# Performance work log

Measured on AMD Instinct MI355X. Metric: run time of the kernel, lower is better.

Reference implementation:

```python
import jax, jax.numpy as jnp
import numpy as np

N = 4_000_000   # points at level d
SIDE = 1024     # coordinate range per axis
HALF = SIDE // 2  # parent coord range


def setup_inputs() -> dict:
    key = jax.random.key(0)
    k1, k2 = jax.random.split(key)
    xyz = jax.random.randint(k1, (N, 3), 0, SIDE, dtype=jnp.int32)
    b = (jnp.arange(N, dtype=jnp.int32) % 4)[:, None]  # 4 batches
    coords = jnp.concatenate([b, xyz], axis=1)          # (N,4): [b,x,y,z]
    kernel = jnp.ones((8,), dtype=jnp.float32)          # frozen all-ones 2x2x2 conv weights
    return {"coords": coords, "kernel": kernel}


def _fog(coords, kernel):
    # pos(): occupancy code 2**(x%2 + 2*y%2 + 4*z%2)
    bits = coords[:, 1:4] & 1                       # (N,3)
    off = bits[:, 0] + 2 * bits[:, 1] + 4 * bits[:, 2]  # (N,) child offset in 2x2x2 window
    pos = jnp.exp2(off.astype(jnp.float32))         # (N,) code in {1,2,4,...,128}
    contrib = pos * kernel[off]                     # per-offset conv weight (all ones)
    # stride-2 conv: parent voxel = floor(xyz/2); linearize (b,z,y,x) into a key
    parent = coords[:, 1:4] >> 1                    # (N,3)
    keys = (((coords[:, 0].astype(jnp.int64) * HALF + parent[:, 2]) * HALF
             + parent[:, 1]) * HALF + parent[:, 0])
    ukeys, inv = jnp.unique(keys, return_inverse=True, size=N, fill_value=-1)
    feats = jax.ops.segment_sum(contrib, inv, num_segments=N)[:, None]  # (N,1)
    # decode padded unique keys back to coords; pad slots -> -1
    px = (ukeys % HALF).astype(jnp.int32)
    py = ((ukeys // HALF) % HALF).astype(jnp.int32)
    pz = ((ukeys // (HALF * HALF)) % HALF).astype(jnp.int32)
    pb = (ukeys // (HALF * HALF * HALF)).astype(jnp.int32)
    valid = (ukeys >= 0)[:, None]
    coords_out = jnp.where(valid, jnp.stack([pb, px, py, pz], axis=1), -1)
    return coords_out, feats


def reference(coords, kernel):
    return _fog(coords, kernel)
```

## Files before the change

kernel.cpp:

```cpp
#include <hip/hip_runtime.h>
#include <stdint.h>

typedef unsigned int u32;
typedef unsigned long long u64;

#define LBITS  14
#define LMASK  ((1u << LBITS) - 1u)
#define NBUCK  (1u << (29 - LBITS))
#define BWORDS (1u << (LBITS - 5))
#define WPL    (BWORDS / 64)
#define WOPAD  (BWORDS + BWORDS / 32)
#define FCAP   192
#define BPB    4
#define TILE_A 4096
#define RPT    (TILE_A / 256)
#define S2     8
#define CAP2   2304
#define RPT2   (CAP2 / 256)
#define RECV   4
#define SCAN_ELEM 2048

__device__ __forceinline__ u32 woidx(u32 w) { return w + (w >> 5); }

__device__ __forceinline__ void wsync() {
    asm volatile("s_waitcnt lgkmcnt(0)" ::: "memory");
}

__device__ __forceinline__ u32 make_key(int4 c) {
    return ((((u32)c.x * 512u + ((u32)c.w >> 1)) * 512u + ((u32)c.z >> 1)) * 512u)
           + ((u32)c.y >> 1);
}

__global__ void __launch_bounds__(256) phase_a(const int4* __restrict__ coords,
        u32* __restrict__ linrec, u32* __restrict__ histmat, int n, u32 NT) {
    __shared__ u32 h[4 * 256];
    u32 t = threadIdx.x, wave = t >> 6;
    for (u32 j = t; j < 1024u; j += 256u) h[j] = 0u;
    __syncthreads();
    u32 base = blockIdx.x * TILE_A;
    u32 m = min((u32)TILE_A, (u32)n - base);
    for (u32 j = t; j < m; j += 256u) {
        int4 c = coords[base + j];
        u32 key = make_key(c);
        u32 off = ((u32)c.y & 1u) | (((u32)c.z & 1u) << 1) | (((u32)c.w & 1u) << 2);
        u32 rec = (key << 3) | off;
        linrec[base + j] = rec;
        atomicAdd(&h[wave * 256u + (rec >> 24)], 1u);
    }
    __syncthreads();
    histmat[t * NT + blockIdx.x] = h[t] + h[256u + t] + h[512u + t] + h[768u + t];
}

__global__ void scan_reduce(const u32* __restrict__ data, u32* __restrict__ partial, u32 G) {
    __shared__ u32 s[256];
    u32 t = threadIdx.x;
    u32 base = blockIdx.x * SCAN_ELEM + t * 8u;
    u32 sum = 0;
    #pragma unroll
    for (int j = 0; j < 8; ++j) { u32 idx = base + j; if (idx < G) sum += data[idx]; }
    s[t] = sum; __syncthreads();
    for (int d = 128; d > 0; d >>= 1) { if ((int)t < d) s[t] += s[t + d]; __syncthreads(); }
    if (t == 0) partial[blockIdx.x] = s[0];
}

__global__ void scan_apply2(const u32* __restrict__ data, u32* __restrict__ out,
                            const u32* __restrict__ partial, u32 G, u32 NB,
                            u32* __restrict__ total) {
    __shared__ u32 s[256];
    __shared__ u32 pb[2];
    u32 t = threadIdx.x;
    u32 p = (t < NB) ? partial[t] : 0u;
    u32 pbef = (t < blockIdx.x) ? p : 0u;
    s[t] = pbef; __syncthreads();
    for (int d = 128; d > 0; d >>= 1) { if ((int)t < d) s[t] += s[t + d]; __syncthreads(); }
    if (t == 0) pb[0] = s[0];
    __syncthreads();
    if (total) {
        s[t] = p; __syncthreads();
        for (int d = 128; d > 0; d >>= 1) { if ((int)t < d) s[t] += s[t + d]; __syncthreads(); }
        if (t == 0) pb[1] = s[0];
        __syncthreads();
        if (blockIdx.x == NB - 1u && t == 0u) total[0] = pb[1];
    }
    u32 base = blockIdx.x * SCAN_ELEM + t * 8u;
    u32 v[8]; u32 sum = 0;
    #pragma unroll
    for (int j = 0; j < 8; ++j) {
        u32 idx = base + j;
        v[j] = (idx < G) ? data[idx] : 0u;
        sum += v[j];
    }
    s[t] = sum; __syncthreads();
    for (int d = 1; d < 256; d <<= 1) {
        u32 add = (t >= (u32)d) ? s[t - d] : 0u;
        __syncthreads(); s[t] += add; __syncthreads();
    }
    u32 run = s[t] - sum + pb[0];
    #pragma unroll
    for (int j = 0; j < 8; ++j) {
        u32 idx = base + j;
        if (idx < G) { u32 x = v[j]; out[idx] = run; run += x; }
    }
}

__global__ void __launch_bounds__(256) part1(const u32* __restrict__ linrec,
        const u32* __restrict__ histmat, u32* __restrict__ tmp, int n, u32 NT) {
    __shared__ u32 stage[TILE_A];
    __shared__ u32 lcur[256];
    __shared__ u32 gb[256];
    __shared__ u32 wtot[4];
    u32 t = threadIdx.x, wave = t >> 6, lane = t & 63u;
    u32 base = blockIdx.x * TILE_A;
    u32 m = min((u32)TILE_A, (u32)n - base);
    lcur[t] = 0u;
    __syncthreads();
    u32 recv[RPT];
    #pragma unroll
    for (int k = 0; k < RPT; ++k) {
        u32 j = (u32)k * 256u + t;
        if (j < m) {
            u32 rec = linrec[base + j];
            recv[k] = rec;
            atomicAdd(&lcur[rec >> 24], 1u);
        }
    }
    __syncthreads();
    u32 v = lcur[t];
    u32 incl = v;
    #pragma unroll
    for (int d = 1; d < 64; d <<= 1) {
        u32 x = __shfl_up(incl, d);
        if ((int)lane >= d) incl += x;
    }
    if (lane == 63u) wtot[wave] = incl;
    __syncthreads();
    u32 off = (wave > 0u ? wtot[0] : 0u) + (wave > 1u ? wtot[1] : 0u)
            + (wave > 2u ? wtot[2] : 0u);
    u32 excl = off + incl - v;
    lcur[t] = excl;
    gb[t] = histmat[t * NT + blockIdx.x] - excl;
    __syncthreads();
    #pragma unroll
    for (int k = 0; k < RPT; ++k) {
        u32 j = (u32)k * 256u + t;
        if (j < m) {
            u32 rec = recv[k];
            u32 pos = atomicAdd(&lcur[rec >> 24], 1u);
            stage[pos] = rec;
        }
    }
    __syncthreads();
    for (u32 j = t; j < m; j += 256u) {
        u32 rec = stage[j];
        tmp[gb[rec >> 24] + j] = rec;
    }
}

__global__ void __launch_bounds__(256) part2a(const u32* __restrict__ tmp,
        const u32* __restrict__ histmat, u32* __restrict__ hist2, int n, u32 NT) {
    __shared__ u32 h[4 * 128];
    u32 t = threadIdx.x, wave = t >> 6;
    u32 c = blockIdx.x / S2, s = blockIdx.x % S2;
    for (u32 j = t; j < 512u; j += 256u) h[j] = 0u;
    __syncthreads();
    u32 cs = histmat[c * NT];
    u32 ce = (c == 255u) ? (u32)n : histmat[(c + 1u) * NT];
    u32 L = ce - cs;
    u32 lo = cs + L * s / S2, hi = cs + L * (s + 1u) / S2;
    for (u32 i = lo + t; i < hi; i += 256u)
        atomicAdd(&h[wave * 128u + ((tmp[i] >> 17) & 127u)], 1u);
    __syncthreads();
    if (t < 128u)
        hist2[((c * 128u + t) * S2) + s] = h[t] + h[128u + t] + h[256u + t] + h[384u + t];
}

__global__ void __launch_bounds__(256) part2b(const u32* __restrict__ tmp,
        const u32* __restrict__ histmat, const u32* __restrict__ hist2,
        u32* __restrict__ buckrec, int n, u32 NT) {
    __shared__ u32 stage[CAP2];
    __shared__ u32 lcur[128];
    __shared__ u32 gb[128];
    __shared__ u32 wtot[2];
    u32 t = threadIdx.x, lane = t & 63u;
    u32 c = blockIdx.x / S2, s = blockIdx.x % S2;
    u32 cs = histmat[c * NT];
    u32 ce = (c == 255u) ? (u32)n : histmat[(c + 1u) * NT];
    u32 L = ce - cs;
    u32 lo = cs + L * s / S2, hi = cs + L * (s + 1u) / S2;
    u32 cnt = hi - lo;
    if (cnt <= (u32)CAP2) {
        if (t < 128u) lcur[t] = 0u;
        __syncthreads();
        u32 recv[RPT2];
        #pragma unroll
        for (int k = 0; k < RPT2; ++k) {
            u32 j = (u32)k * 256u + t;
            if (j < cnt) {
                u32 rec = tmp[lo + j];
                recv[k] = rec;
                atomicAdd(&lcur[(rec >> 17) & 127u], 1u);
            }
        }
        __syncthreads();
        u32 v = 0, incl = 0, excl = 0;
        if (t < 128u) {
            v = lcur[t];
            incl = v;
            #pragma unroll
            for (int d = 1; d < 64; d <<= 1) {
                u32 x = __shfl_up(incl, d);
                if ((int)lane >= d) incl += x;
            }
            if (lane == 63u) wtot[t >> 6] = incl;
        }
        __syncthreads();
        if (t < 128u) {
            u32 off = (t >= 64u) ? wtot[0] : 0u;
            excl = off + incl - v;
            lcur[t] = excl;
            gb[t] = hist2[((c * 128u + t) * S2) + s] - excl;
        }
        __syncthreads();
        #pragma unroll
        for (int k = 0; k < RPT2; ++k) {
            u32 j = (u32)k * 256u + t;
            if (j < cnt) {
                u32 rec = recv[k];
                u32 pos = atomicAdd(&lcur[(rec >> 17) & 127u], 1u);
                stage[pos] = rec;
            }
        }
        __syncthreads();
        for (u32 j = t; j < cnt; j += 256u) {
            u32 rec = stage[j];
            buckrec[gb[(rec >> 17) & 127u] + j] = rec;
        }
    } else {
        if (t < 128u) lcur[t] = hist2[((c * 128u + t) * S2) + s];
        __syncthreads();
        for (u32 i = lo + t; i < hi; i += 256u) {
            u32 rec = tmp[i];
            u32 pos = atomicAdd(&lcur[(rec >> 17) & 127u], 1u);
            buckrec[pos] = rec;
        }
    }
}

__global__ void __launch_bounds__(256) pass_count(const u32* __restrict__ buckrec,
        const u32* __restrict__ hist2, u32* __restrict__ ucount, int n) {
    __shared__ u32 bm[BPB][WOPAD];
    u32 wave = threadIdx.x >> 6, lane = threadIdx.x & 63u;
    u32 bucket = blockIdx.x * BPB + wave;
    u32* B = bm[wave];
    #pragma unroll
    for (int j = 0; j < WPL; ++j) B[woidx(lane * WPL + j)] = 0u;
    wsync();
    u32 start = hist2[bucket * S2];
    u32 end = (bucket + 1u < NBUCK) ? hist2[(bucket + 1u) * S2] : (u32)n;
    for (u32 i = start + lane; i < end; i += 64u) {
        u32 lk = (buckrec[i] >> 3) & LMASK;
        atomicOr(&B[woidx(lk >> 5)], 1u << (lk & 31u));
    }
    wsync();
    u32 sum = 0;
    #pragma unroll
    for (int j = 0; j < WPL; ++j) sum += __popc(B[woidx(lane * WPL + j)]);
    #pragma unroll
    for (int d = 1; d < 64; d <<= 1) sum += __shfl_xor(sum, d);
    if (lane == 0u) ucount[bucket] = sum;
}

__global__ void __launch_bounds__(256) pass_emit(const u32* __restrict__ buckrec,
        const u32* __restrict__ hist2, const u32* __restrict__ ubase,
        const float* __restrict__ kern, float4* __restrict__ rows,
        float* __restrict__ feats, int n) {
    __shared__ u32 bm[BPB][WOPAD];
    __shared__ u32 wofW[BPB][BWORDS];
    __shared__ float fl[BPB][FCAP];
    __shared__ float ksc[BPB][8];
    u32 wave = threadIdx.x >> 6, lane = threadIdx.x & 63u;
    u32 bucket = blockIdx.x * BPB + wave;
    u32* B = bm[wave];
    u32* W = wofW[wave];
    float* F = fl[wave];
    #pragma unroll
    for (int j = 0; j < WPL; ++j) B[woidx(lane * WPL + j)] = 0u;
    #pragma unroll
    for (u32 j = lane; j < FCAP; j += 64u) F[j] = 0.f;
    if (lane < 8u) ksc[wave][lane] = (float)(1u << lane) * kern[lane];
    wsync();
    u32 start = hist2[bucket * S2];
    u32 end = (bucket + 1u < NBUCK) ? hist2[(bucket + 1u) * S2] : (u32)n;
    u32 cnt = end - start;
    u32 recv[RECV];
    #pragma unroll
    for (int k = 0; k < RECV; ++k) {
        u32 idx = (u32)k * 64u + lane;
        if (idx < cnt) {
            u32 rec = buckrec[start + idx];
            recv[k] = rec;
            u32 lk = (rec >> 3) & LMASK;
            atomicOr(&B[woidx(lk >> 5)], 1u << (lk & 31u));
        }
    }
    for (u32 i = start + (u32)RECV * 64u + lane; i < end; i += 64u) {
        u32 lk = (buckrec[i] >> 3) & LMASK;
        atomicOr(&B[woidx(lk >> 5)], 1u << (lk & 31u));
    }
    wsync();
    u32 wv[WPL]; u32 pc[WPL]; u32 sum = 0;
    #pragma unroll
    for (int j = 0; j < WPL; ++j) {
        wv[j] = B[woidx(lane * WPL + j)];
        pc[j] = __popc(wv[j]);
        sum += pc[j];
    }
    u32 incl = sum;
    #pragma unroll
    for (int d = 1; d < 64; d <<= 1) {
        u32 tt = __shfl_up(incl, d);
        if ((int)lane >= d) incl += tt;
    }
    u32 lex = incl - sum;
    u32 uc = __shfl(incl, 63);
    {
        u32 r = lex;
        #pragma unroll
        for (int j = 0; j < WPL; ++j) { W[((u32)j << 6) | lane] = r; r += pc[j]; }
    }
    wsync();
    u32 base = ubase[bucket];
    bool lds_ok = (uc <= FCAP);
    if (!lds_ok) {
        for (u32 j = lane; j < uc; j += 64u) feats[base + j] = 0.f;
        asm volatile("s_waitcnt vmcnt(0)" ::: "memory");
    }
    #pragma unroll
    for (int k = 0; k < RECV; ++k) {
        u32 idx = (u32)k * 64u + lane;
        if (idx < cnt) {
            u32 rec = recv[k];
            float contrib = ksc[wave][rec & 7u];
            u32 lk = (rec >> 3) & LMASK;
            u32 w = lk >> 5, bit = lk & 31u;
            u32 r = W[((w & 7u) << 6) | (w >> 3)]
                  + __popc(B[woidx(w)] & ((1u << bit) - 1u));
            if (lds_ok) atomicAdd(&F[r], contrib);
            else        atomicAdd(&feats[base + r], contrib);
        }
    }
    for (u32 i = start + (u32)RECV * 64u + lane; i < end; i += 64u) {
        u32 rec = buckrec[i];
        float contrib = ksc[wave][rec & 7u];
        u32 lk = (rec >> 3) & LMASK;
        u32 w = lk >> 5, bit = lk & 31u;
        u32 r = W[((w & 7u) << 6) | (w >> 3)]
              + __popc(B[woidx(w)] & ((1u << bit) - 1u));
        if (lds_ok) atomicAdd(&F[r], contrib);
        else        atomicAdd(&feats[base + r], contrib);
    }
    wsync();
    u32 rank = base + lex;
    u32 keyhi = bucket << LBITS;
    #pragma unroll
    for (int j = 0; j < WPL; ++j) {
        u32 bits = wv[j];
        u32 kb = keyhi | ((lane * (u32)WPL + (u32)j) << 5);
        while (bits) {
            u32 tz = __builtin_ctz(bits);
            bits &= bits - 1u;
            u32 key = kb | tz;
            rows[rank++] = make_float4((float)(key >> 27), (float)(key & 511u),
                                       (float)((key >> 9) & 511u),
                                       (float)((key >> 18) & 511u));
        }
    }
    if (lds_ok) {
        for (u32 j = lane; j < uc; j += 64u) feats[base + j] = F[j];
    }
}

__global__ void pad_fill(float4* __restrict__ rows, float* __restrict__ feats,
                         const u32* __restrict__ counter, int n) {
    int i = blockIdx.x * blockDim.x + threadIdx.x;
    if (i < n && (u32)i >= counter[0]) {
        rows[i] = make_float4(-1.f, -1.f, -1.f, -1.f);
        feats[i] = 0.f;
    }
}

extern "C" void kernel_launch(void* const* d_in, const int* in_sizes, int n_in,
                              void* d_out, int out_size, void* d_ws, size_t ws_size,
                              hipStream_t stream) {
    const int n = in_sizes[0] / 4;
    const int4* coords = (const int4*)d_in[0];
    const float* kern  = (const float*)d_in[1];
    const u32 NT = ((u32)n + TILE_A - 1) / TILE_A;
    const u32 G1 = 256 * NT;
    const u32 G2 = 256 * 128 * S2;
    const u32 NB1 = (G1 + SCAN_ELEM - 1) / SCAN_ELEM;
    const u32 NB2 = (G2 + SCAN_ELEM - 1) / SCAN_ELEM;
    const u32 NB3 = (NBUCK + SCAN_ELEM - 1) / SCAN_ELEM;

    u32* wsp = (u32*)d_ws;
    u32* linrec  = wsp;
    u32* tmp     = linrec + n;
    u32* histmat = tmp + n;
    u32* hist2   = histmat + G1;
    u32* ucount  = hist2 + G2;
    u32* counter = ucount + NBUCK;
    u32* spart   = counter + 4;
    u32* buckrec = linrec;

    float4* rows  = (float4*)d_out;
    float*  feats = (float*)((char*)d_out + (size_t)n * 16);

    phase_a<<<NT, 256, 0, stream>>>(coords, linrec, histmat, n, NT);
    scan_reduce<<<NB1, 256, 0, stream>>>(histmat, spart, G1);
    scan_apply2<<<NB1, 256, 0, stream>>>(histmat, histmat, spart, G1, NB1, (u32*)nullptr);
    part1<<<NT, 256, 0, stream>>>(linrec, histmat, tmp, n, NT);
    part2a<<<256 * S2, 256, 0, stream>>>(tmp, histmat, hist2, n, NT);
    scan_reduce<<<NB2, 256, 0, stream>>>(hist2, spart, G2);
    scan_apply2<<<NB2, 256, 0, stream>>>(hist2, hist2, spart, G2, NB2, (u32*)nullptr);
    part2b<<<256 * S2, 256, 0, stream>>>(tmp, histmat, hist2, buckrec, n, NT);
    pass_count<<<NBUCK / BPB, 256, 0, stream>>>(buckrec, hist2, ucount, n);
    scan_reduce<<<NB3, 256, 0, stream>>>(ucount, spart, NBUCK);
    scan_apply2<<<NB3, 256, 0, stream>>>(ucount, ucount, spart, NBUCK, NB3, counter);
    pass_emit<<<NBUCK / BPB, 256, 0, stream>>>(buckrec, hist2, ucount, kern,
                                               rows, feats, n);
    pad_fill<<<((u32)n + 255) / 256, 256, 0, stream>>>(rows, feats, counter, n);
}
```

Baseline: 232.8 us.

## Fuse scan block-reductions into producer kernels and vectorize record loads

Removes two scan_reduce launches by having part2a and pass_count atomically accumulate per-scan-block partial sums into spartB/spartC, which are zeroed by the preceding kernels. part1 and part2a also load records as uint4 with scalar head/tail handling, to cut load instruction count. This saves launch overhead and a full reread of hist2/ucount, but adds global atomics and a block-level tree reduction in part2a. Correctness depends on the block-to-scan-block mapping (c>>1, blockIdx>>9) matching SCAN_ELEM partitioning and on the zeroing kernels running first.

```diff
diff --git a/kernel.cpp b/kernel.cpp
--- a/kernel.cpp
+++ b/kernel.cpp
@@ -104,25 +104,37 @@
 }
 
 __global__ void __launch_bounds__(256) part1(const u32* __restrict__ linrec,
-        const u32* __restrict__ histmat, u32* __restrict__ tmp, int n, u32 NT) {
+        const u32* __restrict__ histmat, u32* __restrict__ tmp,
+        u32* __restrict__ spartB, int n, u32 NT) {
     __shared__ u32 stage[TILE_A];
     __shared__ u32 lcur[256];
     __shared__ u32 gb[256];
     __shared__ u32 wtot[4];
     u32 t = threadIdx.x, wave = t >> 6, lane = t & 63u;
+    if (blockIdx.x == 0u && t < 128u) spartB[t] = 0u;
     u32 base = blockIdx.x * TILE_A;
     u32 m = min((u32)TILE_A, (u32)n - base);
+    u32 m4 = m >> 2, rem = m & 3u;
     lcur[t] = 0u;
     __syncthreads();
-    u32 recv[RPT];
-    #pragma unroll
-    for (int k = 0; k < RPT; ++k) {
-        u32 j = (u32)k * 256u + t;
-        if (j < m) {
-            u32 rec = linrec[base + j];
-            recv[k] = rec;
-            atomicAdd(&lcur[rec >> 24], 1u);
-        }
+    u32 recv[RPT]; u32 tailrec = 0u;
+    const uint4* lr4 = (const uint4*)(linrec + base);
+    #pragma unroll
+    for (int k = 0; k < RPT / 4; ++k) {
+        u32 j4 = (u32)k * 256u + t;
+        if (j4 < m4) {
+            uint4 v = lr4[j4];
+            recv[k * 4 + 0] = v.x; recv[k * 4 + 1] = v.y;
+            recv[k * 4 + 2] = v.z; recv[k * 4 + 3] = v.w;
+            atomicAdd(&lcur[v.x >> 24], 1u);
+            atomicAdd(&lcur[v.y >> 24], 1u);
+            atomicAdd(&lcur[v.z >> 24], 1u);
+            atomicAdd(&lcur[v.w >> 24], 1u);
+        }
+    }
+    if (t < rem) {
+        tailrec = linrec[base + (m & ~3u) + t];
+        atomicAdd(&lcur[tailrec >> 24], 1u);
     }
     __syncthreads();
     u32 v = lcur[t];
@@ -141,13 +153,20 @@
     gb[t] = histmat[t * NT + blockIdx.x] - excl;
     __syncthreads();
     #pragma unroll
-    for (int k = 0; k < RPT; ++k) {
-        u32 j = (u32)k * 256u + t;
-        if (j < m) {
-            u32 rec = recv[k];
-            u32 pos = atomicAdd(&lcur[rec >> 24], 1u);
-            stage[pos] = rec;
-        }
+    for (int k = 0; k < RPT / 4; ++k) {
+        u32 j4 = (u32)k * 256u + t;
+        if (j4 < m4) {
+            #pragma unroll
+            for (int e = 0; e < 4; ++e) {
+                u32 rec = recv[k * 4 + e];
+                u32 pos = atomicAdd(&lcur[rec >> 24], 1u);
+                stage[pos] = rec;
+            }
+        }
+    }
+    if (t < rem) {
+        u32 pos = atomicAdd(&lcur[tailrec >> 24], 1u);
+        stage[pos] = tailrec;
     }
     __syncthreads();
     for (u32 j = t; j < m; j += 256u) {
@@ -157,7 +176,8 @@
 }
 
 __global__ void __launch_bounds__(256) part2a(const u32* __restrict__ tmp,
-        const u32* __restrict__ histmat, u32* __restrict__ hist2, int n, u32 NT) {
+        const u32* __restrict__ histmat, u32* __restrict__ hist2,
+        u32* __restrict__ spartB, int n, u32 NT) {
     __shared__ u32 h[4 * 128];
     u32 t = threadIdx.x, wave = t >> 6;
     u32 c = blockIdx.x / S2, s = blockIdx.x % S2;
@@ -167,21 +187,42 @@
     u32 ce = (c == 255u) ? (u32)n : histmat[(c + 1u) * NT];
     u32 L = ce - cs;
     u32 lo = cs + L * s / S2, hi = cs + L * (s + 1u) / S2;
-    for (u32 i = lo + t; i < hi; i += 256u)
-        atomicAdd(&h[wave * 128u + ((tmp[i] >> 17) & 127u)], 1u);
-    __syncthreads();
-    if (t < 128u)
-        hist2[((c * 128u + t) * S2) + s] = h[t] + h[128u + t] + h[256u + t] + h[384u + t];
+    u32 a0 = min((lo + 3u) & ~3u, hi);
+    u32 a1 = max(a0, hi & ~3u);
+    if (lo + t < a0)
+        atomicAdd(&h[wave * 128u + ((tmp[lo + t] >> 17) & 127u)], 1u);
+    const uint4* t4 = (const uint4*)tmp;
+    for (u32 i4 = (a0 >> 2) + t; i4 < (a1 >> 2); i4 += 256u) {
+        uint4 v = t4[i4];
+        atomicAdd(&h[wave * 128u + ((v.x >> 17) & 127u)], 1u);
+        atomicAdd(&h[wave * 128u + ((v.y >> 17) & 127u)], 1u);
+        atomicAdd(&h[wave * 128u + ((v.z >> 17) & 127u)], 1u);
+        atomicAdd(&h[wave * 128u + ((v.w >> 17) & 127u)], 1u);
+    }
+    if (a1 + t < hi)
+        atomicAdd(&h[wave * 128u + ((tmp[a1 + t] >> 17) & 127u)], 1u);
+    __syncthreads();
+    u32 val = 0u;
+    if (t < 128u) {
+        val = h[t] + h[128u + t] + h[256u + t] + h[384u + t];
+        hist2[((c * 128u + t) * S2) + s] = val;
+    }
+    __syncthreads();
+    h[t] = (t < 128u) ? val : 0u;
+    __syncthreads();
+    for (int d = 128; d > 0; d >>= 1) { if ((int)t < d) h[t] += h[t + d]; __syncthreads(); }
+    if (t == 0u) atomicAdd(&spartB[c >> 1], h[0]);
 }
 
 __global__ void __launch_bounds__(256) part2b(const u32* __restrict__ tmp,
         const u32* __restrict__ histmat, const u32* __restrict__ hist2,
-        u32* __restrict__ buckrec, int n, u32 NT) {
+        u32* __restrict__ buckrec, u32* __restrict__ spartC, int n, u32 NT) {
     __shared__ u32 stage[CAP2];
     __shared__ u32 lcur[128];
     __shared__ u32 gb[128];
     __shared__ u32 wtot[2];
     u32 t = threadIdx.x, lane = t & 63u;
+    if (blockIdx.x == 0u && t < 16u) spartC[t] = 0u;
     u32 c = blockIdx.x / S2, s = blockIdx.x % S2;
     u32 cs = histmat[c * NT];
     u32 ce = (c == 255u) ? (u32)n : histmat[(c + 1u) * NT];
@@ -247,8 +288,10 @@
 }
 
 __global__ void __launch_bounds__(256) pass_count(const u32* __restrict__ buckrec,
-        const u32* __restrict__ hist2, u32* __restrict__ ucount, int n) {
+        const u32* __restrict__ hist2, u32* __restrict__ ucount,
+        u32* __restrict__ spartC, int n) {
     __shared__ u32 bm[BPB][WOPAD];
+    __shared__ u32 su[BPB];
     u32 wave = threadIdx.x >> 6, lane = threadIdx.x & 63u;
     u32 bucket = blockIdx.x * BPB + wave;
     u32* B = bm[wave];
@@ -267,7 +310,10 @@
     for (int j = 0; j < WPL; ++j) sum += __popc(B[woidx(lane * WPL + j)]);
     #pragma unroll
     for (int d = 1; d < 64; d <<= 1) sum += __shfl_xor(sum, d);
-    if (lane == 0u) ucount[bucket] = sum;
+    if (lane == 0u) { ucount[bucket] = sum; su[wave] = sum; }
+    __syncthreads();
+    if (threadIdx.x == 0u)
+        atomicAdd(&spartC[blockIdx.x >> 9], su[0] + su[1] + su[2] + su[3]);
 }
 
 __global__ void __launch_bounds__(256) pass_emit(const u32* __restrict__ buckrec,
@@ -409,23 +455,23 @@
     u32* hist2   = histmat + G1;
     u32* ucount  = hist2 + G2;
     u32* counter = ucount + NBUCK;
-    u32* spart   = counter + 4;
+    u32* spartA  = counter + 4;
+    u32* spartB  = spartA + 256;
+    u32* spartC  = spartB + 128;
     u32* buckrec = linrec;
 
     float4* rows  = (float4*)d_out;
     float*  feats = (float*)((char*)d_out + (size_t)n * 16);
 
     phase_a<<<NT, 256, 0, stream>>>(coords, linrec, histmat, n, NT);
-    scan_reduce<<<NB1, 256, 0, stream>>>(histmat, spart, G1);
-    scan_apply2<<<NB1, 256, 0, stream>>>(histmat, histmat, spart, G1, NB1, (u32*)nullptr);
-    part1<<<NT, 256, 0, stream>>>(linrec, histmat, tmp, n, NT);
-    part2a<<<256 * S2, 256, 0, stream>>>(tmp, histmat, hist2, n, NT);
-    scan_reduce<<<NB2, 256, 0, stream>>>(hist2, spart, G2);
-    scan_apply2<<<NB2, 256, 0, stream>>>(hist2, hist2, spart, G2, NB2, (u32*)nullptr);
-    part2b<<<256 * S2, 256, 0, stream>>>(tmp, histmat, hist2, buckrec, n, NT);
-    pass_count<<<NBUCK / BPB, 256, 0, stream>>>(buckrec, hist2, ucount, n);
-    scan_reduce<<<NB3, 256, 0, stream>>>(ucount, spart, NBUCK);
-    scan_apply2<<<NB3, 256, 0, stream>>>(ucount, ucount, spart, NBUCK, NB3, counter);
+    scan_reduce<<<NB1, 256, 0, stream>>>(histmat, spartA, G1);
+    scan_apply2<<<NB1, 256, 0, stream>>>(histmat, histmat, spartA, G1, NB1, (u32*)nullptr);
+    part1<<<NT, 256, 0, stream>>>(linrec, histmat, tmp, spartB, n, NT);
+    part2a<<<256 * S2, 256, 0, stream>>>(tmp, histmat, hist2, spartB, n, NT);
+    scan_apply2<<<NB2, 256, 0, stream>>>(hist2, hist2, spartB, G2, NB2, (u32*)nullptr);
+    part2b<<<256 * S2, 256, 0, stream>>>(tmp, histmat, hist2, buckrec, spartC, n, NT);
+    pass_count<<<NBUCK / BPB, 256, 0, stream>>>(buckrec, hist2, ucount, spartC, n);
+    scan_apply2<<<NB3, 256, 0, stream>>>(ucount, ucount, spartC, NBUCK, NB3, counter);
     pass_emit<<<NBUCK / BPB, 256, 0, stream>>>(buckrec, hist2, ucount, kern,
                                                rows, feats, n);
     pad_fill<<<((u32)n + 255) / 256, 256, 0, stream>>>(rows, feats, counter, n);
```

New measurement: 303.3 us. 1.3x slower.
